# Performance work log

Measured on AMD Instinct MI355X. Metric: run time of the kernel, lower is better.

Reference implementation:

```python
import jax, jax.numpy as jnp
import numpy as np

N_NODES = 150000       # original nodes
N_FRAG_NODES = 300000  # nodes duplicated across fragments
N_FRAGS = 30000        # number of fragments (segments of fragments_batch)
E = 1200000            # edges in combined fragment graph
D = 128                # nhid


def seg_mean(x, seg, num):
    s = jax.ops.segment_sum(x, seg, num_segments=num)
    c = jax.ops.segment_sum(jnp.ones((x.shape[0], 1), x.dtype), seg, num_segments=num)
    return s / jnp.maximum(c, 1.0)


def setup_inputs() -> dict:
    key = jax.random.key(0)
    ks = jax.random.split(key, 8)
    x = jax.random.normal(ks[0], (N_NODES, D), dtype=jnp.float32)
    mapper = jax.random.randint(ks[1], (N_FRAG_NODES,), 0, N_NODES)
    batch = jnp.sort(jax.random.randint(ks[2], (N_FRAG_NODES,), 0, N_FRAGS))
    edge_index = jax.random.randint(ks[3], (2, E), 0, N_FRAG_NODES)
    W_u = jax.random.normal(ks[4], (D, D), dtype=jnp.float32) * 0.05
    b_u = jnp.zeros((D,), dtype=jnp.float32)
    W_gcn = jax.random.normal(ks[5], (D, D), dtype=jnp.float32) * 0.05
    b_gcn = jnp.zeros((D,), dtype=jnp.float32)
    return {
        "x": x,
        "fragments_nodes_mapper": mapper,
        "fragments_batch": batch,
        "edge_index": edge_index,
        "W_u": W_u,
        "b_u": b_u,
        "W_gcn": W_gcn,
        "b_gcn": b_gcn,
        "i": 0,
    }


def gcn_conv(x, edge_index, W, b, n):
    # PyG GCNConv: add self loops, symmetric normalization D^-1/2 (A+I) D^-1/2, then linear.
    xw = x @ W  # [n, D]
    loops = jnp.arange(n, dtype=edge_index.dtype)
    row = jnp.concatenate([edge_index[0], loops])  # source
    col = jnp.concatenate([edge_index[1], loops])  # target (aggregation index)
    deg = jax.ops.segment_sum(jnp.ones(row.shape[0], x.dtype), col, num_segments=n)
    dinv = jnp.where(deg > 0, jax.lax.rsqrt(jnp.maximum(deg, 1.0)), 0.0)
    norm = dinv[row] * dinv[col]  # [E+n]
    msg = xw[row] * norm[:, None]
    out = jax.ops.segment_sum(msg, col, num_segments=n)
    return out + b


def reference(x, fragments_nodes_mapper, fragments_batch, edge_index, W_u, b_u, W_gcn, b_gcn, i):
    if i == 0:
        x = x[fragments_nodes_mapper]  # gather: [N_FRAG_NODES, D]
    # fragment-level mean pooling, broadcast back to fragment-nodes
    fragment = seg_mean(x, fragments_batch, N_FRAGS)[fragments_batch]
    # U[i-1]: MLP(nhid, nhid, nlayer=1, with_final_activation=True) -> Linear + ReLU
    x = x + jax.nn.relu(fragment @ W_u + b_u)
    # pool duplicated fragment-nodes back onto original nodes, then re-broadcast
    x = seg_mean(x, fragments_nodes_mapper, N_NODES)[fragments_nodes_mapper]
    # GCN over the combined fragment graph
    x = gcn_conv(x, edge_index, W_gcn, b_gcn, N_FRAG_NODES)
    fragment_x = seg_mean(x, fragments_batch, N_FRAGS)  # [N_FRAGS, D]
    return (fragment_x, x)
```

## Files before the change

kernel.cpp:

```cpp
#include <hip/hip_runtime.h>
#include <hip/hip_bf16.h>

#define N_NODES      150000
#define N_FRAG_NODES 300000
#define N_FRAGS      30000
#define NEDGE        1200000
#define D            128
#define DV           32
#define DU           32
#define SCAN_TILE    1024

typedef __attribute__((ext_vector_type(8))) short short8;
typedef __attribute__((ext_vector_type(4))) float f32x4;

__device__ __forceinline__ unsigned short f2bf(float f) {
    unsigned u = __float_as_uint(f);
    u = (u + 0x7FFFu + ((u >> 16) & 1u)) >> 16;
    return (unsigned short)u;
}
__device__ __forceinline__ float bf2f(unsigned short u) {
    return __uint_as_float((unsigned)u << 16);
}

__global__ void k_starts(const int* __restrict__ batch, int* __restrict__ startb) {
    int b = blockIdx.x * blockDim.x + threadIdx.x;
    if (b > N_FRAGS) return;
    int lo = 0, hi = N_FRAG_NODES;
    while (lo < hi) { int mid = (lo + hi) >> 1; if (batch[mid] < b) lo = mid + 1; else hi = mid; }
    startb[b] = lo;
}

__global__ void k_frag_mean(const float* __restrict__ x, const int* __restrict__ mapper,
                            const int* __restrict__ startb, ushort4* __restrict__ frag16) {
    int g = threadIdx.x >> 5, lane = threadIdx.x & 31;
    int b = blockIdx.x * 8 + g;
    if (b >= N_FRAGS) return;
    const float4* x4 = (const float4*)x;
    int s = startb[b], e = startb[b + 1];
    float4 sum = {0.f, 0.f, 0.f, 0.f};
    for (int j = s; j < e; ++j) {
        int m = mapper[j];
        float4 v = x4[(size_t)m * DV + lane];
        sum.x += v.x; sum.y += v.y; sum.z += v.z; sum.w += v.w;
    }
    float c = (float)(e - s); if (c < 1.f) c = 1.f;
    float inv = 1.f / c;
    ushort4 r = {f2bf(sum.x * inv), f2bf(sum.y * inv), f2bf(sum.z * inv), f2bf(sum.w * inv)};
    frag16[(size_t)b * DU + lane] = r;
}

__global__ void k_build_wfrag(const float* __restrict__ W, short* __restrict__ wfrag) {
    int t = threadIdx.x;
    for (int e = t; e < 2048; e += 256) {
        int nt = e >> 8;
        int kk = (e >> 6) & 3;
        int lane = e & 63;
        int col = nt * 16 + (lane & 15);
        int kb = kk * 32 + ((lane >> 4) << 3);
        short8 v;
        #pragma unroll
        for (int j = 0; j < 8; ++j) v[j] = (short)f2bf(W[(kb + j) * D + col]);
        ((short8*)wfrag)[e] = v;
    }
}

template <bool RELU, bool BIAS>
__global__ void __launch_bounds__(256)
k_rowmat_mfma(const unsigned short* __restrict__ src16, const short* __restrict__ wfrag,
              const float* __restrict__ bias, unsigned short* __restrict__ dst16, int rows) {
    __shared__ short8 wl[2048];
    int tid = threadIdx.x;
    for (int e = tid; e < 2048; e += 256) wl[e] = ((const short8*)wfrag)[e];
    __syncthreads();
    int wv = tid >> 6, lane = tid & 63;
    int lrow = lane & 15;
    int lk8 = (lane >> 4);
    float bv[8];
    #pragma unroll
    for (int nt = 0; nt < 8; ++nt) bv[nt] = BIAS ? bias[nt * 16 + lrow] : 0.f;

    int chunk = blockIdx.x * 64;
    {
        int r = chunk + wv * 16 + lrow;
        short8 af[4];
        if (r < rows) {
            const short8* rowp = (const short8*)(src16 + (size_t)r * D);
            #pragma unroll
            for (int kk = 0; kk < 4; ++kk) af[kk] = rowp[kk * 4 + lk8];
        } else {
            #pragma unroll
            for (int kk = 0; kk < 4; ++kk) af[kk] = (short8)0;
        }
        f32x4 acc[8];
        #pragma unroll
        for (int nt = 0; nt < 8; ++nt) acc[nt] = (f32x4)0.f;
        #pragma unroll
        for (int nt = 0; nt < 8; ++nt) {
            #pragma unroll
            for (int kk = 0; kk < 4; ++kk)
                acc[nt] = __builtin_amdgcn_mfma_f32_16x16x32_bf16(
                              af[kk], wl[(nt * 4 + kk) * 64 + lane], acc[nt], 0, 0, 0);
        }
        int orow0 = chunk + wv * 16 + ((lane >> 4) << 2);
        #pragma unroll
        for (int nt = 0; nt < 8; ++nt) {
            int col = nt * 16 + lrow;
            #pragma unroll
            for (int reg = 0; reg < 4; ++reg) {
                int orow = orow0 + reg;
                if (orow < rows) {
                    float v = acc[nt][reg] + bv[nt];
                    if (RELU) v = fmaxf(v, 0.f);
                    dst16[(size_t)orow * D + col] = f2bf(v);
                }
            }
        }
    }
}

__global__ void k_hist(const int* __restrict__ idx, int n, int* __restrict__ cnt) {
    int i = blockIdx.x * blockDim.x + threadIdx.x;
    if (i < n) atomicAdd(&cnt[idx[i]], 1);
}

__global__ void k_scan_tile(const int* __restrict__ cnt, int n, int* __restrict__ starts,
                            int* __restrict__ tsum) {
    __shared__ int buf[SCAN_TILE];
    int tid = threadIdx.x;
    int i = blockIdx.x * SCAN_TILE + tid;
    int v = (i < n) ? cnt[i] : 0;
    buf[tid] = v;
    __syncthreads();
    for (int off = 1; off < SCAN_TILE; off <<= 1) {
        int t = (tid >= off) ? buf[tid - off] : 0;
        __syncthreads();
        buf[tid] += t;
        __syncthreads();
    }
    if (i < n) starts[i] = buf[tid] - v;
    if (tid == SCAN_TILE - 1) tsum[blockIdx.x] = buf[tid];
}

__global__ void k_scan_tsum(int* __restrict__ tsum, int ntiles, int* __restrict__ starts, int n) {
    __shared__ int buf[SCAN_TILE];
    int tid = threadIdx.x;
    int v = (tid < ntiles) ? tsum[tid] : 0;
    buf[tid] = v;
    __syncthreads();
    for (int off = 1; off < SCAN_TILE; off <<= 1) {
        int t = (tid >= off) ? buf[tid - off] : 0;
        __syncthreads();
        buf[tid] += t;
        __syncthreads();
    }
    if (tid < ntiles) tsum[tid] = buf[tid] - v;
    if (tid == SCAN_TILE - 1) starts[n] = buf[tid];
}

__global__ void k_scan_add(int* __restrict__ starts, int n, const int* __restrict__ tsum) {
    int i = blockIdx.x * blockDim.x + threadIdx.x;
    if (i < n) starts[i] += tsum[i >> 10];
}

__global__ void k_fill_m(const int* __restrict__ mapper, const int* __restrict__ batch,
                         const int* __restrict__ starts, int* __restrict__ cnt,
                         int* __restrict__ mvals) {
    int i = blockIdx.x * blockDim.x + threadIdx.x;
    if (i >= N_FRAG_NODES) return;
    int k = mapper[i];
    int pos = atomicSub(&cnt[k], 1) - 1;
    mvals[starts[k] + pos] = batch[i];
}

__global__ void k_dinv(const int* __restrict__ cstart, float* __restrict__ dinv) {
    int c = blockIdx.x * blockDim.x + threadIdx.x;
    if (c >= N_FRAG_NODES) return;
    float deg = (float)(cstart[c + 1] - cstart[c] + 1);
    dinv[c] = rsqrtf(deg);
}

__global__ void k_fill_e(const int* __restrict__ erow, const int* __restrict__ ecol,
                         const int* __restrict__ mapper, const float* __restrict__ dinv,
                         const int* __restrict__ starts, int* __restrict__ cnt,
                         int2* __restrict__ erecs) {
    int i = blockIdx.x * blockDim.x + threadIdx.x;
    if (i >= NEDGE) return;
    int c = ecol[i], r = erow[i];
    int pos = atomicSub(&cnt[c], 1) - 1;
    int2 rec;
    rec.x = mapper[r];
    rec.y = __float_as_int(dinv[r]);
    erecs[starts[c] + pos] = rec;
}

__global__ void k_pool_csr(const float* __restrict__ x, const ushort4* __restrict__ fragu16,
                           const int* __restrict__ mstart, const int* __restrict__ mvals,
                           ushort4* __restrict__ pooled16) {
    int g = threadIdx.x >> 5, lane = threadIdx.x & 31;
    int n = blockIdx.x * 8 + g;
    if (n >= N_NODES) return;
    int s = mstart[n], e = mstart[n + 1];
    ushort4 out = {0, 0, 0, 0};
    if (e > s) {
        float4 sum = {0.f, 0.f, 0.f, 0.f};
        for (int t = s; t < e; ++t) {
            int b = mvals[t];
            ushort4 u = fragu16[(size_t)b * DU + lane];
            sum.x += bf2f(u.x); sum.y += bf2f(u.y); sum.z += bf2f(u.z); sum.w += bf2f(u.w);
        }
        float inv = 1.f / (float)(e - s);
        float4 xv = ((const float4*)x)[(size_t)n * DV + lane];
        out.x = f2bf(xv.x + sum.x * inv); out.y = f2bf(xv.y + sum.y * inv);
        out.z = f2bf(xv.z + sum.z * inv); out.w = f2bf(xv.w + sum.w * inv);
    }
    pooled16[(size_t)n * DU + lane] = out;
}

__global__ void k_gcn_gather(const int* __restrict__ mapper, const int* __restrict__ cstart,
                             const int2* __restrict__ erecs, const ushort4* __restrict__ pw16,
                             const float* __restrict__ dinv, const float* __restrict__ bgcn,
                             float* __restrict__ xout) {
    int g = threadIdx.x >> 5, lane = threadIdx.x & 31;
    int c = blockIdx.x * 8 + g;
    if (c >= N_FRAG_NODES) return;
    int s = cstart[c], e = cstart[c + 1];
    float4 acc = {0.f, 0.f, 0.f, 0.f};
    for (int t = s; t < e; ++t) {
        int2 rec = erecs[t];
        float w = __int_as_float(rec.y);
        ushort4 u = pw16[(size_t)rec.x * DU + lane];
        acc.x = fmaf(bf2f(u.x), w, acc.x); acc.y = fmaf(bf2f(u.y), w, acc.y);
        acc.z = fmaf(bf2f(u.z), w, acc.z); acc.w = fmaf(bf2f(u.w), w, acc.w);
    }
    float dc = dinv[c];
    float dc2 = dc * dc;
    ushort4 su = pw16[(size_t)mapper[c] * DU + lane];
    float4 bg = ((const float4*)bgcn)[lane];
    float4 o;
    o.x = fmaf(acc.x, dc, fmaf(bf2f(su.x), dc2, bg.x));
    o.y = fmaf(acc.y, dc, fmaf(bf2f(su.y), dc2, bg.y));
    o.z = fmaf(acc.z, dc, fmaf(bf2f(su.z), dc2, bg.z));
    o.w = fmaf(acc.w, dc, fmaf(bf2f(su.w), dc2, bg.w));
    ((float4*)xout)[(size_t)c * DV + lane] = o;
}

__global__ void k_frag_x(const float* __restrict__ xout, const int* __restrict__ startb,
                         float* __restrict__ fout) {
    int g = threadIdx.x >> 5, lane = threadIdx.x & 31;
    int b = blockIdx.x * 8 + g;
    if (b >= N_FRAGS) return;
    const float4* x4 = (const float4*)xout;
    int s = startb[b], e = startb[b + 1];
    float4 sum = {0.f, 0.f, 0.f, 0.f};
    for (int j = s; j < e; ++j) {
        float4 v = x4[(size_t)j * DV + lane];
        sum.x += v.x; sum.y += v.y; sum.z += v.z; sum.w += v.w;
    }
    float4 r = {0.f, 0.f, 0.f, 0.f};
    if (e > s) {
        float inv = 1.f / (float)(e - s);
        r.x = sum.x * inv; r.y = sum.y * inv; r.z = sum.z * inv; r.w = sum.w * inv;
    }
    ((float4*)fout)[(size_t)b * DV + lane] = r;
}

static inline void run_scan(const int* cnt, int n, int* starts, int* tsum, hipStream_t stream) {
    int ntiles = (n + SCAN_TILE - 1) / SCAN_TILE;
    k_scan_tile<<<ntiles, SCAN_TILE, 0, stream>>>(cnt, n, starts, tsum);
    k_scan_tsum<<<1, SCAN_TILE, 0, stream>>>(tsum, ntiles, starts, n);
    k_scan_add<<<(n + 255) / 256, 256, 0, stream>>>(starts, n, tsum);
}

extern "C" void kernel_launch(void* const* d_in, const int* in_sizes, int n_in,
                              void* d_out, int out_size, void* d_ws, size_t ws_size,
                              hipStream_t stream) {
    const float* x      = (const float*)d_in[0];
    const int*   mapper = (const int*)d_in[1];
    const int*   batch  = (const int*)d_in[2];
    const int*   erow   = (const int*)d_in[3];
    const int*   ecol   = erow + NEDGE;
    const float* W_u    = (const float*)d_in[4];
    const float* b_u    = (const float*)d_in[5];
    const float* W_gcn  = (const float*)d_in[6];
    const float* b_gcn  = (const float*)d_in[7];

    float* fout = (float*)d_out;
    float* xout = fout + (size_t)N_FRAGS * D;

    short*  wfragU   = (short*)d_ws;
    short*  wfragG   = wfragU + 16384;
    int2*   erecs    = (int2*)(wfragG + 16384);
    unsigned short* frag16   = (unsigned short*)(erecs + NEDGE);
    unsigned short* pooled16 = frag16 + (size_t)N_FRAGS * D;
    float*  dinv   = (float*)(pooled16 + (size_t)N_NODES * D);
    int*    startb = (int*)(dinv + N_FRAG_NODES);
    int*    mstart = startb + (N_FRAGS + 1);
    int*    cstart = mstart + (N_NODES + 1);
    int*    mcnt   = cstart + (N_FRAG_NODES + 1);
    int*    ccnt   = mcnt + N_NODES;
    int*    mvals  = ccnt + N_FRAG_NODES;
    int*    tsum   = mvals + N_FRAG_NODES;

    hipMemsetAsync(mcnt, 0, (size_t)(N_NODES + N_FRAG_NODES) * sizeof(int), stream);

    k_build_wfrag<<<1, 256, 0, stream>>>(W_u, wfragU);
    k_build_wfrag<<<1, 256, 0, stream>>>(W_gcn, wfragG);

    k_starts<<<(N_FRAGS + 256) / 256, 256, 0, stream>>>(batch, startb);
    k_frag_mean<<<(N_FRAGS + 7) / 8, 256, 0, stream>>>(x, mapper, startb, (ushort4*)frag16);
    k_rowmat_mfma<true, true><<<(N_FRAGS + 63) / 64, 256, 0, stream>>>(
        frag16, wfragU, b_u, frag16, N_FRAGS);

    k_hist<<<(N_FRAG_NODES + 255) / 256, 256, 0, stream>>>(mapper, N_FRAG_NODES, mcnt);
    run_scan(mcnt, N_NODES, mstart, tsum, stream);
    k_fill_m<<<(N_FRAG_NODES + 255) / 256, 256, 0, stream>>>(mapper, batch, mstart, mcnt, mvals);

    k_pool_csr<<<(N_NODES + 7) / 8, 256, 0, stream>>>(x, (const ushort4*)frag16,
                                                      mstart, mvals, (ushort4*)pooled16);
    k_rowmat_mfma<false, false><<<(N_NODES + 63) / 64, 256, 0, stream>>>(
        pooled16, wfragG, nullptr, pooled16, N_NODES);

    k_hist<<<(NEDGE + 255) / 256, 256, 0, stream>>>(ecol, NEDGE, ccnt);
    run_scan(ccnt, N_FRAG_NODES, cstart, tsum, stream);
    k_dinv<<<(N_FRAG_NODES + 255) / 256, 256, 0, stream>>>(cstart, dinv);
    k_fill_e<<<(NEDGE + 255) / 256, 256, 0, stream>>>(erow, ecol, mapper, dinv, cstart, ccnt, erecs);

    k_gcn_gather<<<(N_FRAG_NODES + 7) / 8, 256, 0, stream>>>(mapper, cstart, erecs,
                                                             (const ushort4*)pooled16,
                                                             dinv, b_gcn, xout);
    k_frag_x<<<(N_FRAGS + 7) / 8, 256, 0, stream>>>(xout, startb, fout);
}
```

Before: 430.4 us.

## Fuse histograms and scans, drop dinv kernel, widen gather vectors and unroll

Merges the two histogram passes and the batch-start binary search into a single prep kernel, then runs one combined prefix scan over both count arrays. This cuts the number of kernel launches and separate passes. The dinv buffer and its kernel are removed, and degree normalisation is recomputed inline from cstart. The pool and GCN gather kernels move to 16 lanes per row with 16-byte bf16 loads, and the gather/mean loops are unrolled by two with dual accumulators to expose more memory-level parallelism.

```diff
diff --git a/kernel.cpp b/kernel.cpp
--- a/kernel.cpp
+++ b/kernel.cpp
@@ -5,12 +5,13 @@
 #define N_FRAG_NODES 300000
 #define N_FRAGS      30000
 #define NEDGE        1200000
+#define NCNT         (N_NODES + N_FRAG_NODES)
 #define D            128
 #define DV           32
-#define DU           32
 #define SCAN_TILE    1024
 
 typedef __attribute__((ext_vector_type(8))) short short8;
+typedef __attribute__((ext_vector_type(8))) unsigned short u16x8;
 typedef __attribute__((ext_vector_type(4))) float f32x4;
 
 __device__ __forceinline__ unsigned short f2bf(float f) {
@@ -22,31 +23,91 @@
     return __uint_as_float((unsigned)u << 16);
 }
 
-__global__ void k_starts(const int* __restrict__ batch, int* __restrict__ startb) {
-    int b = blockIdx.x * blockDim.x + threadIdx.x;
-    if (b > N_FRAGS) return;
-    int lo = 0, hi = N_FRAG_NODES;
-    while (lo < hi) { int mid = (lo + hi) >> 1; if (batch[mid] < b) lo = mid + 1; else hi = mid; }
-    startb[b] = lo;
-}
-
-__global__ void k_frag_mean(const float* __restrict__ x, const int* __restrict__ mapper,
+__global__ void k_prep(const int* __restrict__ mapper, const int* __restrict__ batch,
+                       const int* __restrict__ ecol, int* __restrict__ mcnt,
+                       int* __restrict__ ccnt, int* __restrict__ startb) {
+    int i = blockIdx.x * blockDim.x + threadIdx.x;
+    if (i < NEDGE) atomicAdd(&ccnt[ecol[i]], 1);
+    if (i < N_FRAG_NODES) atomicAdd(&mcnt[mapper[i]], 1);
+    if (i <= N_FRAGS) {
+        int lo = 0, hi = N_FRAG_NODES;
+        while (lo < hi) { int mid = (lo + hi) >> 1; if (batch[mid] < i) lo = mid + 1; else hi = mid; }
+        startb[i] = lo;
+    }
+}
+
+__global__ void k_scan_tile(const int* __restrict__ cnt, int* __restrict__ combst,
+                            int* __restrict__ tsum) {
+    __shared__ int buf[SCAN_TILE];
+    int tid = threadIdx.x;
+    int i = blockIdx.x * SCAN_TILE + tid;
+    int v = (i < NCNT) ? cnt[i] : 0;
+    buf[tid] = v;
+    __syncthreads();
+    for (int off = 1; off < SCAN_TILE; off <<= 1) {
+        int t = (tid >= off) ? buf[tid - off] : 0;
+        __syncthreads();
+        buf[tid] += t;
+        __syncthreads();
+    }
+    if (i < NCNT) combst[i] = buf[tid] - v;
+    if (tid == SCAN_TILE - 1) tsum[blockIdx.x] = buf[tid];
+}
+
+__global__ void k_scan_tsum(int* __restrict__ tsum, int ntiles,
+                            int* __restrict__ mstart, int* __restrict__ cstart) {
+    __shared__ int buf[SCAN_TILE];
+    int tid = threadIdx.x;
+    int v = (tid < ntiles) ? tsum[tid] : 0;
+    buf[tid] = v;
+    __syncthreads();
+    for (int off = 1; off < SCAN_TILE; off <<= 1) {
+        int t = (tid >= off) ? buf[tid - off] : 0;
+        __syncthreads();
+        buf[tid] += t;
+        __syncthreads();
+    }
+    if (tid < ntiles) tsum[tid] = buf[tid] - v;
+    if (tid == SCAN_TILE - 1) {
+        mstart[N_NODES] = N_FRAG_NODES;
+        cstart[N_FRAG_NODES] = buf[tid] - N_FRAG_NODES;
+    }
+}
+
+__global__ void k_scan_add(const int* __restrict__ combst, const int* __restrict__ tsum,
+                           int* __restrict__ mstart, int* __restrict__ cstart) {
+    int i = blockIdx.x * blockDim.x + threadIdx.x;
+    if (i >= NCNT) return;
+    int v = combst[i] + tsum[i >> 10];
+    if (i < N_NODES) mstart[i] = v;
+    else cstart[i - N_NODES] = v - N_FRAG_NODES;
+}
+
+__global__ void k_frag_mean(const float4* __restrict__ x4, const int* __restrict__ mapper,
                             const int* __restrict__ startb, ushort4* __restrict__ frag16) {
     int g = threadIdx.x >> 5, lane = threadIdx.x & 31;
     int b = blockIdx.x * 8 + g;
     if (b >= N_FRAGS) return;
-    const float4* x4 = (const float4*)x;
     int s = startb[b], e = startb[b + 1];
-    float4 sum = {0.f, 0.f, 0.f, 0.f};
-    for (int j = s; j < e; ++j) {
-        int m = mapper[j];
-        float4 v = x4[(size_t)m * DV + lane];
-        sum.x += v.x; sum.y += v.y; sum.z += v.z; sum.w += v.w;
+    float4 sA = {0.f, 0.f, 0.f, 0.f}, sB = {0.f, 0.f, 0.f, 0.f};
+    int j = s;
+    for (; j + 2 <= e; j += 2) {
+        int m0 = mapper[j], m1 = mapper[j + 1];
+        float4 v0 = x4[(size_t)m0 * DV + lane];
+        float4 v1 = x4[(size_t)m1 * DV + lane];
+        sA.x += v0.x; sA.y += v0.y; sA.z += v0.z; sA.w += v0.w;
+        sB.x += v1.x; sB.y += v1.y; sB.z += v1.z; sB.w += v1.w;
+    }
+    if (j < e) {
+        int m0 = mapper[j];
+        float4 v0 = x4[(size_t)m0 * DV + lane];
+        sA.x += v0.x; sA.y += v0.y; sA.z += v0.z; sA.w += v0.w;
     }
     float c = (float)(e - s); if (c < 1.f) c = 1.f;
     float inv = 1.f / c;
-    ushort4 r = {f2bf(sum.x * inv), f2bf(sum.y * inv), f2bf(sum.z * inv), f2bf(sum.w * inv)};
-    frag16[(size_t)b * DU + lane] = r;
+    ushort4 r = {f2bf((sA.x + sB.x) * inv), f2bf((sA.y + sB.y) * inv),
+                 f2bf((sA.z + sB.z) * inv), f2bf((sA.w + sB.w) * inv)};
+    frag16[(size_t)b * DV + lane] = r;
 }
 
 __global__ void k_build_wfrag(const float* __restrict__ W, short* __restrict__ wfrag) {
@@ -118,157 +179,148 @@
     }
 }
 
-__global__ void k_hist(const int* __restrict__ idx, int n, int* __restrict__ cnt) {
-    int i = blockIdx.x * blockDim.x + threadIdx.x;
-    if (i < n) atomicAdd(&cnt[idx[i]], 1);
-}
-
-__global__ void k_scan_tile(const int* __restrict__ cnt, int n, int* __restrict__ starts,
-                            int* __restrict__ tsum) {
-    __shared__ int buf[SCAN_TILE];
-    int tid = threadIdx.x;
-    int i = blockIdx.x * SCAN_TILE + tid;
-    int v = (i < n) ? cnt[i] : 0;
-    buf[tid] = v;
-    __syncthreads();
-    for (int off = 1; off < SCAN_TILE; off <<= 1) {
-        int t = (tid >= off) ? buf[tid - off] : 0;
-        __syncthreads();
-        buf[tid] += t;
-        __syncthreads();
-    }
-    if (i < n) starts[i] = buf[tid] - v;
-    if (tid == SCAN_TILE - 1) tsum[blockIdx.x] = buf[tid];
-}
-
-__global__ void k_scan_tsum(int* __restrict__ tsum, int ntiles, int* __restrict__ starts, int n) {
-    __shared__ int buf[SCAN_TILE];
-    int tid = threadIdx.x;
-    int v = (tid < ntiles) ? tsum[tid] : 0;
-    buf[tid] = v;
-    __syncthreads();
-    for (int off = 1; off < SCAN_TILE; off <<= 1) {
-        int t = (tid >= off) ? buf[tid - off] : 0;
-        __syncthreads();
-        buf[tid] += t;
-        __syncthreads();
-    }
-    if (tid < ntiles) tsum[tid] = buf[tid] - v;
-    if (tid == SCAN_TILE - 1) starts[n] = buf[tid];
-}
-
-__global__ void k_scan_add(int* __restrict__ starts, int n, const int* __restrict__ tsum) {
-    int i = blockIdx.x * blockDim.x + threadIdx.x;
-    if (i < n) starts[i] += tsum[i >> 10];
-}
-
 __global__ void k_fill_m(const int* __restrict__ mapper, const int* __restrict__ batch,
-                         const int* __restrict__ starts, int* __restrict__ cnt,
+                         const int* __restrict__ mstart, int* __restrict__ mcnt,
                          int* __restrict__ mvals) {
     int i = blockIdx.x * blockDim.x + threadIdx.x;
     if (i >= N_FRAG_NODES) return;
     int k = mapper[i];
-    int pos = atomicSub(&cnt[k], 1) - 1;
-    mvals[starts[k] + pos] = batch[i];
-}
-
-__global__ void k_dinv(const int* __restrict__ cstart, float* __restrict__ dinv) {
-    int c = blockIdx.x * blockDim.x + threadIdx.x;
-    if (c >= N_FRAG_NODES) return;
-    float deg = (float)(cstart[c + 1] - cstart[c] + 1);
-    dinv[c] = rsqrtf(deg);
+    int pos = atomicSub(&mcnt[k], 1) - 1;
+    mvals[mstart[k] + pos] = batch[i];
 }
 
 __global__ void k_fill_e(const int* __restrict__ erow, const int* __restrict__ ecol,
-                         const int* __restrict__ mapper, const float* __restrict__ dinv,
-                         const int* __restrict__ starts, int* __restrict__ cnt,
-                         int2* __restrict__ erecs) {
+                         const int* __restrict__ mapper, const int* __restrict__ cstart,
+                         int* __restrict__ ccnt, int2* __restrict__ erecs) {
     int i = blockIdx.x * blockDim.x + threadIdx.x;
     if (i >= NEDGE) return;
     int c = ecol[i], r = erow[i];
-    int pos = atomicSub(&cnt[c], 1) - 1;
+    int pos = atomicSub(&ccnt[c], 1) - 1;
+    float w = rsqrtf((float)(cstart[r + 1] - cstart[r] + 1));
     int2 rec;
     rec.x = mapper[r];
-    rec.y = __float_as_int(dinv[r]);
-    erecs[starts[c] + pos] = rec;
-}
-
-__global__ void k_pool_csr(const float* __restrict__ x, const ushort4* __restrict__ fragu16,
+    rec.y = __float_as_int(w);
+    erecs[cstart[c] + pos] = rec;
+}
+
+__global__ void k_pool_csr(const float4* __restrict__ x4, const u16x8* __restrict__ fragu8,
                            const int* __restrict__ mstart, const int* __restrict__ mvals,
-                           ushort4* __restrict__ pooled16) {
-    int g = threadIdx.x >> 5, lane = threadIdx.x & 31;
-    int n = blockIdx.x * 8 + g;
+                           u16x8* __restrict__ pooled8) {
+    int g = threadIdx.x >> 4, lane = threadIdx.x & 15;
+    int n = blockIdx.x * 16 + g;
     if (n >= N_NODES) return;
     int s = mstart[n], e = mstart[n + 1];
-    ushort4 out = {0, 0, 0, 0};
+    u16x8 out = (u16x8)0;
     if (e > s) {
-        float4 sum = {0.f, 0.f, 0.f, 0.f};
-        for (int t = s; t < e; ++t) {
-            int b = mvals[t];
-            ushort4 u = fragu16[(size_t)b * DU + lane];
-            sum.x += bf2f(u.x); sum.y += bf2f(u.y); sum.z += bf2f(u.z); sum.w += bf2f(u.w);
+        float accA[8], accB[8];
+        #pragma unroll
+        for (int j = 0; j < 8; ++j) { accA[j] = 0.f; accB[j] = 0.f; }
+        int t = s;
+        for (; t + 2 <= e; t += 2) {
+            int b0 = mvals[t], b1 = mvals[t + 1];
+            u16x8 u0 = fragu8[(size_t)b0 * 16 + lane];
+            u16x8 u1 = fragu8[(size_t)b1 * 16 + lane];
+            #pragma unroll
+            for (int j = 0; j < 8; ++j) {
+                accA[j] += bf2f(u0[j]);
+                accB[j] += bf2f(u1[j]);
+            }
+        }
+        if (t < e) {
+            int b0 = mvals[t];
+            u16x8 u0 = fragu8[(size_t)b0 * 16 + lane];
+            #pragma unroll
+            for (int j = 0; j < 8; ++j) accA[j] += bf2f(u0[j]);
         }
         float inv = 1.f / (float)(e - s);
-        float4 xv = ((const float4*)x)[(size_t)n * DV + lane];
-        out.x = f2bf(xv.x + sum.x * inv); out.y = f2bf(xv.y + sum.y * inv);
-        out.z = f2bf(xv.z + sum.z * inv); out.w = f2bf(xv.w + sum.w * inv);
-    }
-    pooled16[(size_t)n * DU + lane] = out;
+        float4 xv0 = x4[(size_t)n * DV + lane * 2];
+        float4 xv1 = x4[(size_t)n * DV + lane * 2 + 1];
+        out[0] = f2bf(fmaf(accA[0] + accB[0], inv, xv0.x));
+        out[1] = f2bf(fmaf(accA[1] + accB[1], inv, xv0.y));
+        out[2] = f2bf(fmaf(accA[2] + accB[2], inv, xv0.z));
+        out[3] = f2bf(fmaf(accA[3] + accB[3], inv, xv0.w));
+        out[4] = f2bf(fmaf(accA[4] + accB[4], inv, xv1.x));
+        out[5] = f2bf(fmaf(accA[5] + accB[5], inv, xv1.y));
+        out[6] = f2bf(fmaf(accA[6] + accB[6], inv, xv1.z));
+        out[7] = f2bf(fmaf(accA[7] + accB[7], inv, xv1.w));
+    }
+    pooled8[(size_t)n * 16 + lane] = out;
 }
 
 __global__ void k_gcn_gather(const int* __restrict__ mapper, const int* __restrict__ cstart,
-                             const int2* __restrict__ erecs, const ushort4* __restrict__ pw16,
-                             const float* __restrict__ dinv, const float* __restrict__ bgcn,
-                             float* __restrict__ xout) {
-    int g = threadIdx.x >> 5, lane = threadIdx.x & 31;
-    int c = blockIdx.x * 8 + g;
+                             const int2* __restrict__ erecs, const u16x8* __restrict__ pw8,
+                             const float* __restrict__ bgcn, float4* __restrict__ xout4) {
+    int g = threadIdx.x >> 4, lane = threadIdx.x & 15;
+    int c = blockIdx.x * 16 + g;
     if (c >= N_FRAG_NODES) return;
     int s = cstart[c], e = cstart[c + 1];
-    float4 acc = {0.f, 0.f, 0.f, 0.f};
-    for (int t = s; t < e; ++t) {
-        int2 rec = erecs[t];
-        float w = __int_as_float(rec.y);
-        ushort4 u = pw16[(size_t)rec.x * DU + lane];
-        acc.x = fmaf(bf2f(u.x), w, acc.x); acc.y = fmaf(bf2f(u.y), w, acc.y);
-        acc.z = fmaf(bf2f(u.z), w, acc.z); acc.w = fmaf(bf2f(u.w), w, acc.w);
-    }
-    float dc = dinv[c];
+    float dc = rsqrtf((float)(e - s + 1));
+    float accA[8], accB[8];
+    #pragma unroll
+    for (int j = 0; j < 8; ++j) { accA[j] = 0.f; accB[j] = 0.f; }
+    int t = s;
+    for (; t + 2 <= e; t += 2) {
+        int2 r0 = erecs[t];
+        int2 r1 = erecs[t + 1];
+        u16x8 u0 = pw8[(size_t)r0.x * 16 + lane];
+        u16x8 u1 = pw8[(size_t)r1.x * 16 + lane];
+        float w0 = __int_as_float(r0.y);
+        float w1 = __int_as_float(r1.y);
+        #pragma unroll
+        for (int j = 0; j < 8; ++j) {
+            accA[j] = fmaf(bf2f(u0[j]), w0, accA[j]);
+            accB[j] = fmaf(bf2f(u1[j]), w1, accB[j]);
+        }
+    }
+    if (t < e) {
+        int2 r0 = erecs[t];
+        u16x8 u0 = pw8[(size_t)r0.x * 16 + lane];
+        float w0 = __int_as_float(r0.y);
+        #pragma unroll
+        for (int j = 0; j < 8; ++j) accA[j] = fmaf(bf2f(u0[j]), w0, accA[j]);
+    }
+    u16x8 su = pw8[(size_t)mapper[c] * 16 + lane];
     float dc2 = dc * dc;
-    ushort4 su = pw16[(size_t)mapper[c] * DU + lane];
-    float4 bg = ((const float4*)bgcn)[lane];
-    float4 o;
-    o.x = fmaf(acc.x, dc, fmaf(bf2f(su.x), dc2, bg.x));
-    o.y = fmaf(acc.y, dc, fmaf(bf2f(su.y), dc2, bg.y));
-    o.z = fmaf(acc.z, dc, fmaf(bf2f(su.z), dc2, bg.z));
-    o.w = fmaf(acc.w, dc, fmaf(bf2f(su.w), dc2, bg.w));
-    ((float4*)xout)[(size_t)c * DV + lane] = o;
-}
-
-__global__ void k_frag_x(const float* __restrict__ xout, const int* __restrict__ startb,
-                         float* __restrict__ fout) {
+    const float4* bg4 = (const float4*)bgcn;
+    float4 b0 = bg4[lane * 2], b1 = bg4[lane * 2 + 1];
+    float4 o0, o1;
+    o0.x = fmaf(accA[0] + accB[0], dc, fmaf(bf2f(su[0]), dc2, b0.x));
+    o0.y = fmaf(accA[1] + accB[1], dc, fmaf(bf2f(su[1]), dc2, b0.y));
+    o0.z = fmaf(accA[2] + accB[2], dc, fmaf(bf2f(su[2]), dc2, b0.z));
+    o0.w = fmaf(accA[3] + accB[3], dc, fmaf(bf2f(su[3]), dc2, b0.w));
+    o1.x = fmaf(accA[4] + accB[4], dc, fmaf(bf2f(su[4]), dc2, b1.x));
+    o1.y = fmaf(accA[5] + accB[5], dc, fmaf(bf2f(su[5]), dc2, b1.y));
+    o1.z = fmaf(accA[6] + accB[6], dc, fmaf(bf2f(su[6]), dc2, b1.z));
+    o1.w = fmaf(accA[7] + accB[7], dc, fmaf(bf2f(su[7]), dc2, b1.w));
+    xout4[(size_t)c * DV + lane * 2] = o0;
+    xout4[(size_t)c * DV + lane * 2 + 1] = o1;
+}
+
+__global__ void k_frag_x(const float4* __restrict__ x4, const int* __restrict__ startb,
+                         float4* __restrict__ fout4) {
     int g = threadIdx.x >> 5, lane = threadIdx.x & 31;
     int b = blockIdx.x * 8 + g;
     if (b >= N_FRAGS) return;
-    const float4* x4 = (const float4*)xout;
     int s = startb[b], e = startb[b + 1];
-    float4 sum = {0.f, 0.f, 0.f, 0.f};
-    for (int j = s; j < e; ++j) {
-        float4 v = x4[(size_t)j * DV + lane];
-        sum.x += v.x; sum.y += v.y; sum.z += v.z; sum.w += v.w;
+    float4 sA = {0.f, 0.f, 0.f, 0.f}, sB = {0.f, 0.f, 0.f, 0.f};
+    int j = s;
+    for (; j + 2 <= e; j += 2) {
+        float4 v0 = x4[(size_t)j * DV + lane];
+        float4 v1 = x4[(size_t)(j + 1) * DV + lane];
+        sA.x += v0.x; sA.y += v0.y; sA.z += v0.z; sA.w += v0.w;
+        sB.x += v1.x; sB.y += v1.y; sB.z += v1.z; sB.w += v1.w;
+    }
+    if (j < e) {
+        float4 v0 = x4[(size_t)j * DV + lane];
+        sA.x += v0.x; sA.y += v0.y; sA.z += v0.z; sA.w += v0.w;
     }
     float4 r = {0.f, 0.f, 0.f, 0.f};
     if (e > s) {
         float inv = 1.f / (float)(e - s);
-        r.x = sum.x * inv; r.y = sum.y * inv; r.z = sum.z * inv; r.w = sum.w * inv;
-    }
-    ((float4*)fout)[(size_t)b * DV + lane] = r;
-}
-
-static inline void run_scan(const int* cnt, int n, int* starts, int* tsum, hipStream_t stream) {
-    int ntiles = (n + SCAN_TILE - 1) / SCAN_TILE;
-    k_scan_tile<<<ntiles, SCAN_TILE, 0, stream>>>(cnt, n, starts, tsum);
-    k_scan_tsum<<<1, SCAN_TILE, 0, stream>>>(tsum, ntiles, starts, n);
-    k_scan_add<<<(n + 255) / 256, 256, 0, stream>>>(starts, n, tsum);
+        r.x = (sA.x + sB.x) * inv; r.y = (sA.y + sB.y) * inv;
+        r.z = (sA.z + sB.z) * inv; r.w = (sA.w + sB.w) * inv;
+    }
+    fout4[(size_t)b * DV + lane] = r;
 }
 
 extern "C" void kernel_launch(void* const* d_in, const int* in_sizes, int n_in,
@@ -292,41 +344,42 @@
     int2*   erecs    = (int2*)(wfragG + 16384);
     unsigned short* frag16   = (unsigned short*)(erecs + NEDGE);
     unsigned short* pooled16 = frag16 + (size_t)N_FRAGS * D;
-    float*  dinv   = (float*)(pooled16 + (size_t)N_NODES * D);
-    int*    startb = (int*)(dinv + N_FRAG_NODES);
+    int*    startb = (int*)(pooled16 + (size_t)N_NODES * D);
     int*    mstart = startb + (N_FRAGS + 1);
     int*    cstart = mstart + (N_NODES + 1);
     int*    mcnt   = cstart + (N_FRAG_NODES + 1);
     int*    ccnt   = mcnt + N_NODES;
     int*    mvals  = ccnt + N_FRAG_NODES;
-    int*    tsum   = mvals + N_FRAG_NODES;
-
-    hipMemsetAsync(mcnt, 0, (size_t)(N_NODES + N_FRAG_NODES) * sizeof(int), stream);
+    int*    combst = mvals + N_FRAG_NODES;
+    int*    tsum   = combst + NCNT;
+
+    hipMemsetAsync(mcnt, 0, (size_t)NCNT * sizeof(int), stream);
 
     k_build_wfrag<<<1, 256, 0, stream>>>(W_u, wfragU);
     k_build_wfrag<<<1, 256, 0, stream>>>(W_gcn, wfragG);
 
-    k_starts<<<(N_FRAGS + 256) / 256, 256, 0, stream>>>(batch, startb);
-    k_frag_mean<<<(N_FRAGS + 7) / 8, 256, 0, stream>>>(x, mapper, startb, (ushort4*)frag16);
+    k_prep<<<(NEDGE + 255) / 256, 256, 0, stream>>>(mapper, batch, ecol, mcnt, ccnt, startb);
+
+    int ntiles = (NCNT + SCAN_TILE - 1) / SCAN_TILE;
+    k_scan_tile<<<ntiles, SCAN_TILE, 0, stream>>>(mcnt, combst, tsum);
+    k_scan_tsum<<<1, SCAN_TILE, 0, stream>>>(tsum, ntiles, mstart, cstart);
+    k_scan_add<<<(NCNT + 255) / 256, 256, 0, stream>>>(combst, tsum, mstart, cstart);
+
+    k_frag_mean<<<(N_FRAGS + 7) / 8, 256, 0, stream>>>((const float4*)x, mapper, startb,
+                                                       (ushort4*)frag16);
     k_rowmat_mfma<true, true><<<(N_FRAGS + 63) / 64, 256, 0, stream>>>(
         frag16, wfragU, b_u, frag16, N_FRAGS);
 
-    k_hist<<<(N_FRAG_NODES + 255) / 256, 256, 0, stream>>>(mapper, N_FRAG_NODES, mcnt);
-    run_scan(mcnt, N_NODES, mstart, tsum, stream);
     k_fill_m<<<(N_FRAG_NODES + 255) / 256, 256, 0, stream>>>(mapper, batch, mstart, mcnt, mvals);
-
-    k_pool_csr<<<(N_NODES + 7) / 8, 256, 0, stream>>>(x, (const ushort4*)frag16,
-                                                      mstart, mvals, (ushort4*)pooled16);
+    k_pool_csr<<<(N_NODES + 15) / 16, 256, 0, stream>>>((const float4*)x, (const u16x8*)frag16,
+                                                        mstart, mvals, (u16x8*)pooled16);
     k_rowmat_mfma<false, false><<<(N_NODES + 63) / 64, 256, 0, stream>>>(
         pooled16, wfragG, nullptr, pooled16, N_NODES);
 
-    k_hist<<<(NEDGE + 255) / 256, 256, 0, stream>>>(ecol, NEDGE, ccnt);
-    run_scan(ccnt, N_FRAG_NODES, cstart, tsum, stream);
-    k_dinv<<<(N_FRAG_NODES + 255) / 256, 256, 0, stream>>>(cstart, dinv);
-    k_fill_e<<<(NEDGE + 255) / 256, 256, 0, stream>>>(erow, ecol, mapper, dinv, cstart, ccnt, erecs);
-
-    k_gcn_gather<<<(N_FRAG_NODES + 7) / 8, 256, 0, stream>>>(mapper, cstart, erecs,
-                                                             (const ushort4*)pooled16,
-                                                             dinv, b_gcn, xout);
-    k_frag_x<<<(N_FRAGS + 7) / 8, 256, 0, stream>>>(xout, startb, fout);
-}
+    k_fill_e<<<(NEDGE + 255) / 256, 256, 0, stream>>>(erow, ecol, mapper, cstart, ccnt, erecs);
+
+    k_gcn_gather<<<(N_FRAG_NODES + 15) / 16, 256, 0, stream>>>(mapper, cstart, erecs,
+                                                               (const u16x8*)pooled16,
+                                                               b_gcn, (float4*)xout);
+    k_frag_x<<<(N_FRAGS + 7) / 8, 256, 0, stream>>>((const float4*)xout, startb, (float4*)fout);
+}
```

Result: faster. 366.9 us (-14.7%).
